# Kernel tuning notes

Hardware: AMD Instinct MI355X
Metric: run time of the kernel (lower is better)

## Reference

```python
import jax, jax.numpy as jnp
import numpy as np

R = 32  # voxel resolution

def leaky(x):
    return jnp.where(x > 0, x, 0.1 * x)

def bn(x, gamma, beta, axes, eps=1e-4):
    mu = jnp.mean(x, axis=axes, keepdims=True)
    var = jnp.var(x, axis=axes, keepdims=True)
    shape = [1] * x.ndim
    shape[1] = x.shape[1]
    g = gamma.reshape(shape)
    b = beta.reshape(shape)
    return (x - mu) * jax.lax.rsqrt(var + eps) * g + b

def voxelize(features, coords, r):
    # features: (B, C, N), coords: (B, 3, N)
    B, C, N = features.shape
    mean = jnp.mean(coords, axis=2, keepdims=True)
    norm = (coords - mean + 1.0) / 2.0 * r
    norm = jnp.clip(norm, 0.0, r - 1.0)            # (B, 3, N) continuous voxel coords
    vox = jnp.round(norm).astype(jnp.int32)
    flat = (vox[:, 0] * r + vox[:, 1]) * r + vox[:, 2]      # (B, N)
    seg = (flat + jnp.arange(B, dtype=jnp.int32)[:, None] * (r ** 3)).reshape(-1)
    data = features.transpose(0, 2, 1).reshape(B * N, C)
    sums = jax.ops.segment_sum(data, seg, num_segments=B * r ** 3)
    cnt = jax.ops.segment_sum(jnp.ones((B * N,), data.dtype), seg, num_segments=B * r ** 3)
    avg = sums / jnp.maximum(cnt, 1.0)[:, None]
    grid = avg.reshape(B, r, r, r, C).transpose(0, 4, 1, 2, 3)  # (B, C, r, r, r)
    return grid, norm

def trilinear_devoxelize(grid, norm, r):
    # grid: (B, C, r, r, r), norm: (B, 3, N) in [0, r-1]
    B, C = grid.shape[:2]
    N = norm.shape[2]
    lo = jnp.floor(norm).astype(jnp.int32)
    frac = norm - lo.astype(norm.dtype)
    hi = jnp.minimum(lo + 1, r - 1)
    gf = grid.reshape(B, C, r ** 3)
    out = jnp.zeros((B, C, N), grid.dtype)
    for dx in (0, 1):
        for dy in (0, 1):
            for dz in (0, 1):
                ix = hi[:, 0] if dx else lo[:, 0]
                iy = hi[:, 1] if dy else lo[:, 1]
                iz = hi[:, 2] if dz else lo[:, 2]
                wx = frac[:, 0] if dx else 1.0 - frac[:, 0]
                wy = frac[:, 1] if dy else 1.0 - frac[:, 1]
                wz = frac[:, 2] if dz else 1.0 - frac[:, 2]
                idx = (ix * r + iy) * r + iz                    # (B, N)
                g = jnp.take_along_axis(gf, idx[:, None, :], axis=2)  # (B, C, N)
                out = out + g * (wx * wy * wz)[:, None, :]
    return out

def conv3d(x, w, b):
    y = jax.lax.conv_general_dilated(
        x, w, window_strides=(1, 1, 1), padding=[(1, 1)] * 3,
        dimension_numbers=('NCDHW', 'OIDHW', 'NCDHW'))
    return y + b[None, :, None, None, None]

def setup_inputs() -> dict:
    key = jax.random.key(0)
    ks = jax.random.split(key, 8)
    B, Cin, Cout, N = 8, 64, 64, 32768
    s1 = 1.0 / np.sqrt(Cin * 27)
    s2 = 1.0 / np.sqrt(Cout * 27)
    return {
        'features': jax.random.normal(ks[0], (B, Cin, N), jnp.float32),
        'coords': jax.random.normal(ks[1], (B, 3, N), jnp.float32),
        'conv1_w': jax.random.normal(ks[2], (Cout, Cin, 3, 3, 3), jnp.float32) * s1,
        'conv1_b': jnp.zeros((Cout,), jnp.float32),
        'bn1_g': jnp.ones((Cout,), jnp.float32),
        'bn1_b': jnp.zeros((Cout,), jnp.float32),
        'conv2_w': jax.random.normal(ks[3], (Cout, Cout, 3, 3, 3), jnp.float32) * s2,
        'conv2_b': jnp.zeros((Cout,), jnp.float32),
        'bn2_g': jnp.ones((Cout,), jnp.float32),
        'bn2_b': jnp.zeros((Cout,), jnp.float32),
        'mlp_w': jax.random.normal(ks[4], (Cout, Cin), jnp.float32) / np.sqrt(Cin),
        'mlp_b': jnp.zeros((Cout,), jnp.float32),
        'bnp_g': jnp.ones((Cout,), jnp.float32),
        'bnp_b': jnp.zeros((Cout,), jnp.float32),
    }

def reference(features, coords, conv1_w, conv1_b, bn1_g, bn1_b,
              conv2_w, conv2_b, bn2_g, bn2_b, mlp_w, mlp_b, bnp_g, bnp_b):
    grid, norm = voxelize(features, coords, R)
    v = leaky(bn(conv3d(grid, conv1_w, conv1_b), bn1_g, bn1_b, (0, 2, 3, 4)))
    v = leaky(bn(conv3d(v, conv2_w, conv2_b), bn2_g, bn2_b, (0, 2, 3, 4)))
    sampled = trilinear_devoxelize(v, norm, R)                 # (B, Cout, N)
    p = jnp.einsum('oi,bin->bon', mlp_w, features) + mlp_b[None, :, None]
    p = leaky(bn(p, bnp_g, bnp_b, (0, 2)))
    fused = sampled + p
    return fused, v
```

## Files before the change

### kernel.cpp

```cpp
#include <hip/hip_runtime.h>
#include <hip/hip_bf16.h>

#define BB 8
#define CC 64
#define NPTS 32768
#define RR 32
#define RV 32768
#define MTOT (BB*RV)
#define EPSV 1e-4f

#define OFF_BUFA 0u
#define OFF_BUFB 16777216u
#define OFF_WB1  25165824u
#define OFF_WB2  25221120u
#define OFF_ZG   25276416u
#define OFF_BASE 25276480u
#define OFF_AUX  25800768u
#define OFF_CELL 25801024u
#define OFF_CNT  26063168u
#define OFF_MEAN 26325312u
#define OFF_PART1 26325504u
#define OFF_PART2 26456576u
#define OFF_SCL1 26587648u
#define OFF_SFT1 26587712u
#define OFF_SCL2 26587776u
#define OFF_SFT2 26587840u
#define OFF_WM   26587904u
#define OFF_PARTP 26590208u
#define OFF_SCLP 27114496u
#define OFF_SFTP 27114560u
#define OFF_NORM 33554432u

typedef __attribute__((ext_vector_type(8))) __bf16 bf16x8;
typedef __attribute__((ext_vector_type(8))) unsigned short u16x8;
typedef __attribute__((ext_vector_type(4))) float f32x4;

__device__ __forceinline__ float b2f(ushort u) {
    union { unsigned u; float f; } x; x.u = ((unsigned)u) << 16; return x.f;
}
__device__ __forceinline__ ushort f2b(float f) {
    __hip_bfloat16 h = __float2bfloat16(f);
    return *reinterpret_cast<ushort*>(&h);
}

__global__ void k_coord_mean(const float* __restrict__ coords, float* __restrict__ mean) {
    int ba = blockIdx.x >> 3, ch = blockIdx.x & 7;
    const float* src = coords + (size_t)ba * NPTS + ch * 4096;
    float s = 0.f;
    for (int i = threadIdx.x; i < 4096; i += 256) s += src[i];
    __shared__ float red[256];
    red[threadIdx.x] = s; __syncthreads();
    for (int w = 128; w > 0; w >>= 1) {
        if (threadIdx.x < w) red[threadIdx.x] += red[threadIdx.x + w];
        __syncthreads();
    }
    if (threadIdx.x == 0) atomicAdd(&mean[ba], red[0]);
}

__global__ void k_cellid(const float* __restrict__ coords, const float* __restrict__ mean,
                         float* __restrict__ norm, int* __restrict__ cellid,
                         unsigned* __restrict__ cnt) {
    int idx = blockIdx.x * 256 + threadIdx.x;
    int b = idx >> 15, n = idx & (NPTS - 1);
    int flat = 0;
    #pragma unroll
    for (int a = 0; a < 3; ++a) {
        float c = coords[((size_t)(b * 3 + a)) * NPTS + n];
        float nm = (c - mean[b * 3 + a] * (1.0f / NPTS) + 1.0f) * (0.5f * RR);
        nm = fminf(fmaxf(nm, 0.0f), (float)(RR - 1));
        norm[((size_t)(b * 3 + a)) * NPTS + n] = nm;
        flat = flat * RR + (int)rintf(nm);
    }
    int cell = b * RV + flat;
    cellid[idx] = cell;
    atomicAdd(&cnt[cell], 1u);
}

__global__ void k_scan1(const unsigned* __restrict__ cnt, unsigned* __restrict__ base,
                        unsigned* __restrict__ aux) {
    int tid = threadIdx.x;
    int c0 = blockIdx.x * 1024 + tid * 4;
    unsigned v0 = cnt[c0], v1 = cnt[c0 + 1], v2 = cnt[c0 + 2], v3 = cnt[c0 + 3];
    unsigned tot = v0 + v1 + v2 + v3;
    __shared__ unsigned sc[256];
    sc[tid] = tot; __syncthreads();
    for (int off = 1; off < 256; off <<= 1) {
        unsigned t = (tid >= off) ? sc[tid - off] : 0u;
        __syncthreads();
        sc[tid] += t;
        __syncthreads();
    }
    unsigned excl = sc[tid] - tot;
    base[c0] = excl;
    base[c0 + 1] = excl + v0;
    base[c0 + 2] = excl + v0 + v1;
    base[c0 + 3] = excl + v0 + v1 + v2;
    if (tid == 255) aux[blockIdx.x] = sc[255];
}

__global__ void k_scan2(unsigned* __restrict__ aux) {
    int tid = threadIdx.x;
    unsigned own = aux[tid];
    __shared__ unsigned sc[256];
    sc[tid] = own; __syncthreads();
    for (int off = 1; off < 256; off <<= 1) {
        unsigned t = (tid >= off) ? sc[tid - off] : 0u;
        __syncthreads();
        sc[tid] += t;
        __syncthreads();
    }
    aux[tid] = sc[tid] - own;
}

__global__ void k_scan3(unsigned* __restrict__ base, const unsigned* __restrict__ aux) {
    int i = blockIdx.x * 256 + threadIdx.x;
    base[i] += aux[i >> 10];
}

__global__ __launch_bounds__(256) void k_scatfeat(
    const float* __restrict__ feats, const int* __restrict__ cellid,
    unsigned* __restrict__ base, ushort* __restrict__ fsort,
    const ushort* __restrict__ wmb, const float* __restrict__ mbias,
    ushort* __restrict__ pb, float* __restrict__ partp) {
    __shared__ float t[64 * 65];
    __shared__ unsigned spos[64];
    __shared__ float sf[512];
    int b = blockIdx.x >> 9;
    int n0 = (blockIdx.x & 511) * 64;
    int tid = threadIdx.x;
    #pragma unroll
    for (int k = 0; k < 16; ++k) {
        int idx = k * 256 + tid;
        int c = idx >> 6, nl = idx & 63;
        t[c * 65 + nl] = feats[((size_t)(b * 64 + c)) * NPTS + n0 + nl];
    }
    if (tid < 64) {
        int cell = cellid[(b << 15) + n0 + tid];
        spos[tid] = atomicAdd(&base[cell], 1u);
    }
    __syncthreads();
    #pragma unroll
    for (int it = 0; it < 2; ++it) {
        int pl = it * 32 + (tid >> 3);
        int j = tid & 7;
        unsigned pos = spos[pl];
        u16x8 v;
        #pragma unroll
        for (int k = 0; k < 8; ++k) v[k] = f2b(t[(j * 8 + k) * 65 + pl]);
        *reinterpret_cast<u16x8*>(fsort + (((size_t)pos) << 6) + j * 8) = v;
    }
    int w = tid >> 6, l = tid & 63;
    int nl = l & 15, kg = l >> 4;
    bf16x8 Af[2];
    #pragma unroll
    for (int ks = 0; ks < 2; ++ks) {
        union { u16x8 u; bf16x8 h; } cv;
        #pragma unroll
        for (int j = 0; j < 8; ++j)
            cv.u[j] = f2b(t[(ks * 32 + kg * 8 + j) * 65 + w * 16 + nl]);
        Af[ks] = cv.h;
    }
    f32x4 acc[4];
    #pragma unroll
    for (int cb = 0; cb < 4; ++cb) acc[cb] = (f32x4){0.f, 0.f, 0.f, 0.f};
    #pragma unroll
    for (int ks = 0; ks < 2; ++ks)
        #pragma unroll
        for (int cb = 0; cb < 4; ++cb) {
            bf16x8 Bf = *reinterpret_cast<const bf16x8*>(wmb + (cb * 16 + nl) * 64 + ks * 32 + kg * 8);
            acc[cb] = __builtin_amdgcn_mfma_f32_16x16x32_bf16(Af[ks], Bf, acc[cb], 0, 0, 0);
        }
    float ss[4] = {0.f, 0.f, 0.f, 0.f}, qq[4] = {0.f, 0.f, 0.f, 0.f};
    #pragma unroll
    for (int cb = 0; cb < 4; ++cb) {
        float bsv = mbias[cb * 16 + nl];
        #pragma unroll
        for (int r = 0; r < 4; ++r) {
            float yv = acc[cb][r] + bsv;
            int pt = w * 16 + kg * 4 + r;
            pb[(((size_t)((b << 15) + n0 + pt)) << 6) + cb * 16 + nl] = f2b(yv);
            ss[cb] += yv; qq[cb] += yv * yv;
        }
    }
    #pragma unroll
    for (int cb = 0; cb < 4; ++cb) {
        ss[cb] += __shfl_xor(ss[cb], 16); ss[cb] += __shfl_xor(ss[cb], 32);
        qq[cb] += __shfl_xor(qq[cb], 16); qq[cb] += __shfl_xor(qq[cb], 32);
    }
    if (l < 16) {
        #pragma unroll
        for (int cb = 0; cb < 4; ++cb) {
            sf[w * 128 + cb * 16 + nl] = ss[cb];
            sf[w * 128 + 64 + cb * 16 + nl] = qq[cb];
        }
    }
    __syncthreads();
    if (tid < 128)
        partp[(size_t)tid * 4096 + blockIdx.x] =
            sf[tid] + sf[128 + tid] + sf[256 + tid] + sf[384 + tid];
}

__global__ __launch_bounds__(256) void k_gather(
    const ushort* __restrict__ fsort, const unsigned* __restrict__ base,
    const unsigned* __restrict__ cnt, __hip_bfloat16* __restrict__ xb) {
    int cell = blockIdx.x * 4 + (threadIdx.x >> 6);
    int lane = threadIdx.x & 63;
    unsigned n = cnt[cell];
    unsigned start = base[cell] - n;
    const ushort* rows = fsort + (((size_t)start) << 6) + lane;
    float acc = 0.f;
    unsigned i = 0;
    for (; i + 8 <= n; i += 8) {
        float f0 = b2f(rows[((size_t)(i + 0)) << 6]);
        float f1 = b2f(rows[((size_t)(i + 1)) << 6]);
        float f2 = b2f(rows[((size_t)(i + 2)) << 6]);
        float f3 = b2f(rows[((size_t)(i + 3)) << 6]);
        float f4 = b2f(rows[((size_t)(i + 4)) << 6]);
        float f5 = b2f(rows[((size_t)(i + 5)) << 6]);
        float f6 = b2f(rows[((size_t)(i + 6)) << 6]);
        float f7 = b2f(rows[((size_t)(i + 7)) << 6]);
        acc += ((f0 + f1) + (f2 + f3)) + ((f4 + f5) + (f6 + f7));
    }
    for (; i < n; ++i) acc += b2f(rows[((size_t)i) << 6]);
    float inv = (n > 0) ? (1.0f / (float)n) : 0.f;
    xb[((size_t)cell << 6) + lane] = __float2bfloat16(acc * inv);
}

__global__ void k_wb(const float* __restrict__ w, __hip_bfloat16* __restrict__ wb) {
    int i = blockIdx.x * 256 + threadIdx.x;
    if (i >= CC * CC * 27) return;
    int tap = i % 27, t = i / 27;
    int ci = t & 63, co = t >> 6;
    wb[((size_t)(tap * 64 + co)) * 64 + ci] = __float2bfloat16(w[i]);
}

__global__ void k_wm(const float* __restrict__ w, ushort* __restrict__ wmb) {
    int i = blockIdx.x * 256 + threadIdx.x;
    if (i < 4096) wmb[i] = f2b(w[i]);
}

template<int MODE>
__global__ __launch_bounds__(512, 2) void k_conv_mfma(
    const ushort* __restrict__ src, const ushort* __restrict__ wb,
    const float* __restrict__ bias, const float* __restrict__ scl,
    const float* __restrict__ sft, ushort* __restrict__ y,
    float* __restrict__ part, const ushort* __restrict__ zg) {
    __shared__ __align__(16) char sh[128000 + 32768];
    char* wsh = sh + 128000;
    int tid = threadIdx.x;
    int lane = tid & 63, wid = tid >> 6;
    int tile = ((blockIdx.x & 7) << 6) | (blockIdx.x >> 3);
    int twi = tile & 3, thi = (tile >> 2) & 3;
    int tdi = (tile >> 4) & 3, b = tile >> 6;
    int d0 = tdi * 8, h0 = thi * 8, w0 = twi * 8;

    auto stage_wgt = [&](int g) {
        const ushort* wgrp = wb + g * 8192;
        char* wdst0 = wsh + (g & 1) * 16384;
        #pragma unroll
        for (int i = 0; i < 2; ++i) {
            int idx = i * 8 + wid;
            int c = idx * 64 + lane;
            int row = c >> 3, off = c & 7;
            const ushort* gsrc = wgrp + (((row << 3) + (off ^ (row & 7))) << 3);
            char* ldst = wdst0 + (idx << 10);
            __builtin_amdgcn_global_load_lds(
                (const __attribute__((address_space(1))) void*)gsrc,
                (__attribute__((address_space(3))) void*)ldst, 16, 0, 0);
        }
    };

    float sc8[8], sf8[8];
    if (MODE == 1) {
        int c0 = (lane & 7) * 8;
        #pragma unroll
        for (int j = 0; j < 8; ++j) { sc8[j] = scl[c0 + j]; sf8[j] = sft[c0 + j]; }
    }

    #pragma unroll
    for (int it = 0; it < 16; ++it) {
        int idx = it * 8 + wid;
        if (idx < 125) {
            int c = idx * 64 + lane;
            int row = c >> 3, off = c & 7;
            int dz = row / 100, rem = row - dz * 100;
            int hz = rem / 10, wz = rem - hz * 10;
            int gd = d0 - 1 + dz, gh = h0 - 1 + hz, gw = w0 - 1 + wz;
            bool inb = ((unsigned)gd < 32u) && ((unsigned)gh < 32u) && ((unsigned)gw < 32u);
            if (MODE == 0) {
                int srcoff = off ^ (row & 7);
                const ushort* gsrc = inb
                    ? src + ((((size_t)((b << 15) | (gd << 10) | (gh << 5) | gw)) << 6) + srcoff * 8)
                    : zg;
                char* ldst = sh + (idx << 10);
                __builtin_amdgcn_global_load_lds(
                    (const __attribute__((address_space(1))) void*)gsrc,
                    (__attribute__((address_space(3))) void*)ldst, 16, 0, 0);
            } else {
                u16x8 v = {0, 0, 0, 0, 0, 0, 0, 0};
                if (inb) {
                    v = *reinterpret_cast<const u16x8*>(
                        src + ((((size_t)((b << 15) | (gd << 10) | (gh << 5) | gw)) << 6) + off * 8));
                    #pragma unroll
                    for (int j = 0; j < 8; ++j) {
                        float f = fmaf(b2f(v[j]), sc8[j], sf8[j]);
                        f = f > 0.f ? f : 0.1f * f;
                        v[j] = f2b(f);
                    }
                }
                int la = ((row << 7) + (off << 4)) ^ ((row & 7) << 4);
                *reinterpret_cast<u16x8*>(sh + la) = v;
            }
        }
    }
    stage_wgt(0);

    int nl = lane & 15, kg = lane >> 4;
    int rbase = wid * 100 + (nl >> 3) * 10 + (nl & 7);
    int bswz = (nl & 7) << 4;

    f32x4 acc[4][4];
    #pragma unroll
    for (int mi = 0; mi < 4; ++mi)
        #pragma unroll
        for (int cb = 0; cb < 4; ++cb) acc[mi][cb] = (f32x4){0.f, 0.f, 0.f, 0.f};

    __syncthreads();

    #pragma unroll 1
    for (int g = 0; g < 14; ++g) {
        if (g < 13) stage_wgt(g + 1);
        const char* wlds = wsh + (g & 1) * 16384;
        #pragma unroll
        for (int tl = 0; tl < 2; ++tl) {
            int t = g * 2 + tl;
            if (t < 27) {
                int kd = t / 9, rm = t - kd * 9;
                int kh = rm / 3, kw = rm - kh * 3;
                int rt = rbase + kd * 100 + kh * 10 + kw;
                bf16x8 a[4][2];
                #pragma unroll
                for (int mi = 0; mi < 4; ++mi) {
                    int r = rt + mi * 20;
                    int ba = ((r << 7) + (kg << 4)) ^ ((r & 7) << 4);
                    a[mi][0] = *reinterpret_cast<const bf16x8*>(sh + ba);
                    a[mi][1] = *reinterpret_cast<const bf16x8*>(sh + (ba ^ 64));
                }
                bf16x8 bf[4][2];
                #pragma unroll
                for (int cb = 0; cb < 4; ++cb) {
                    int rowb = tl * 64 + cb * 16 + nl;
                    int bb0 = ((rowb << 7) + (kg << 4)) ^ bswz;
                    bf[cb][0] = *reinterpret_cast<const bf16x8*>(wlds + bb0);
                    bf[cb][1] = *reinterpret_cast<const bf16x8*>(wlds + (bb0 ^ 64));
                }
                __builtin_amdgcn_s_setprio(1);
                #pragma unroll
                for (int ks = 0; ks < 2; ++ks)
                    #pragma unroll
                    for (int mi = 0; mi < 4; ++mi)
                        #pragma unroll
                        for (int cb = 0; cb < 4; ++cb)
                            acc[mi][cb] = __builtin_amdgcn_mfma_f32_16x16x32_bf16(
                                a[mi][ks], bf[cb][ks], acc[mi][cb], 0, 0, 0);
                __builtin_amdgcn_s_setprio(0);
            }
        }
        __syncthreads();
    }

    int d = d0 + wid;
    float bs[4];
    #pragma unroll
    for (int cb = 0; cb < 4; ++cb) bs[cb] = bias[cb * 16 + nl];
    float ss[4] = {0.f, 0.f, 0.f, 0.f}, qq[4] = {0.f, 0.f, 0.f, 0.f};
    #pragma unroll
    for (int mi = 0; mi < 4; ++mi) {
        int h = h0 + mi * 2 + (kg >> 1);
        int w = w0 + (kg & 1) * 4;
        size_t vox = (size_t)((b << 15) | (d << 10) | (h << 5) | w);
        #pragma unroll
        for (int cb = 0; cb < 4; ++cb) {
            int co = cb * 16 + nl;
            #pragma unroll
            for (int r = 0; r < 4; ++r) {
                float yv = acc[mi][cb][r] + bs[cb];
                y[((vox + r) << 6) + co] = f2b(yv);
                ss[cb] += yv; qq[cb] += yv * yv;
            }
        }
    }
    #pragma unroll
    for (int cb = 0; cb < 4; ++cb) {
        ss[cb] += __shfl_xor(ss[cb], 16); ss[cb] += __shfl_xor(ss[cb], 32);
        qq[cb] += __shfl_xor(qq[cb], 16); qq[cb] += __shfl_xor(qq[cb], 32);
    }
    float* sf2 = (float*)sh;
    __syncthreads();
    if (lane < 16) {
        #pragma unroll
        for (int cb = 0; cb < 4; ++cb) {
            sf2[wid * 128 + cb * 16 + nl] = ss[cb];
            sf2[wid * 128 + 64 + cb * 16 + nl] = qq[cb];
        }
    }
    __syncthreads();
    if (tid < 128) {
        float t = sf2[tid] + sf2[128 + tid] + sf2[256 + tid] + sf2[384 + tid]
                + sf2[512 + tid] + sf2[640 + tid] + sf2[768 + tid] + sf2[896 + tid];
        part[tid * 512 + blockIdx.x] = t;
    }
}

__global__ void k_redbn(const float* __restrict__ part, const float* __restrict__ g,
                        const float* __restrict__ bb, float* __restrict__ scl,
                        float* __restrict__ sft, int cnt) {
    int c = blockIdx.x;
    float s = 0.f, q = 0.f;
    for (int i = threadIdx.x; i < cnt; i += 256) {
        s += part[(size_t)c * cnt + i];
        q += part[(size_t)(64 + c) * cnt + i];
    }
    __shared__ float rs[256], rq[256];
    rs[threadIdx.x] = s; rq[threadIdx.x] = q; __syncthreads();
    for (int w = 128; w > 0; w >>= 1) {
        if (threadIdx.x < w) { rs[threadIdx.x] += rs[threadIdx.x + w]; rq[threadIdx.x] += rq[threadIdx.x + w]; }
        __syncthreads();
    }
    if (threadIdx.x == 0) {
        float mu = rs[0] * (1.0f / MTOT);
        float var = rq[0] * (1.0f / MTOT) - mu * mu;
        float sc = g[c] * rsqrtf(var + EPSV);
        scl[c] = sc; sft[c] = bb[c] - mu * sc;
    }
}

__global__ void k_transpose(const ushort* __restrict__ in, const float* __restrict__ scl,
                            const float* __restrict__ sft, float* __restrict__ out) {
    __shared__ float t[64 * 65];
    size_t base = (size_t)blockIdx.x * 4096;
    int gv0 = blockIdx.x * 64;
    int b = gv0 >> 15;
    int vox0 = gv0 & 32767;
    int chl = threadIdx.x & 63;
    float sc = scl[chl], sf = sft[chl];
    #pragma unroll
    for (int k = 0; k < 16; ++k) {
        int idx = k * 256 + threadIdx.x;
        float v = fmaf(b2f(in[base + idx]), sc, sf);
        t[(idx >> 6) * 65 + (idx & 63)] = v > 0.f ? v : 0.1f * v;
    }
    __syncthreads();
    #pragma unroll
    for (int k = 0; k < 16; ++k) {
        int idx = k * 256 + threadIdx.x;
        int ch = idx >> 6, voxl = idx & 63;
        out[((size_t)(b * 64 + ch)) * RV + vox0 + voxl] = t[voxl * 65 + ch];
    }
}

__global__ __launch_bounds__(256) void k_final(
    float* __restrict__ out, const ushort* __restrict__ pbuf,
    const ushort* __restrict__ vraw, const float* __restrict__ norm,
    const float* __restrict__ scl, const float* __restrict__ sft,
    const float* __restrict__ sclp, const float* __restrict__ sftp) {
    __shared__ float smp[64 * 65];
    int b = blockIdx.x >> 9;
    int n0 = (blockIdx.x & 511) * 64;
    int wid = threadIdx.x >> 6, lane = threadIdx.x & 63;
    const ushort* gb = vraw + (((size_t)b) << 15) * CC;
    const float* nrm0 = norm + ((size_t)(b * 3)) * NPTS;
    float sc = scl[lane], sf = sft[lane];
    float scp = sclp[lane], sfp = sftp[lane];

    #pragma unroll 2
    for (int i = 0; i < 16; ++i) {
        int pl = wid * 16 + i;
        int n = n0 + pl;
        float v0 = nrm0[n];
        float v1 = nrm0[NPTS + n];
        float v2 = nrm0[2 * NPTS + n];
        int lx = (int)floorf(v0), ly = (int)floorf(v1), lz = (int)floorf(v2);
        float fx = v0 - (float)lx, fy = v1 - (float)ly, fz = v2 - (float)lz;
        int hx = min(lx + 1, 31), hy = min(ly + 1, 31), hz = min(lz + 1, 31);
        float gx = 1.f - fx, gy = 1.f - fy, gz = 1.f - fz;

        int i000 = ((lx * 32 + ly) * 32 + lz) << 6;
        int i001 = ((lx * 32 + ly) * 32 + hz) << 6;
        int i010 = ((lx * 32 + hy) * 32 + lz) << 6;
        int i011 = ((lx * 32 + hy) * 32 + hz) << 6;
        int i100 = ((hx * 32 + ly) * 32 + lz) << 6;
        int i101 = ((hx * 32 + ly) * 32 + hz) << 6;
        int i110 = ((hx * 32 + hy) * 32 + lz) << 6;
        int i111 = ((hx * 32 + hy) * 32 + hz) << 6;

        float w000 = gx * gy * gz, w001 = gx * gy * fz;
        float w010 = gx * fy * gz, w011 = gx * fy * fz;
        float w100 = fx * gy * gz, w101 = fx * gy * fz;
        float w110 = fx * fy * gz, w111 = fx * fy * fz;

        float r0 = fmaf(b2f(gb[i000 + lane]), sc, sf); r0 = r0 > 0.f ? r0 : 0.1f * r0;
        float r1 = fmaf(b2f(gb[i001 + lane]), sc, sf); r1 = r1 > 0.f ? r1 : 0.1f * r1;
        float r2 = fmaf(b2f(gb[i010 + lane]), sc, sf); r2 = r2 > 0.f ? r2 : 0.1f * r2;
        float r3 = fmaf(b2f(gb[i011 + lane]), sc, sf); r3 = r3 > 0.f ? r3 : 0.1f * r3;
        float r4 = fmaf(b2f(gb[i100 + lane]), sc, sf); r4 = r4 > 0.f ? r4 : 0.1f * r4;
        float r5 = fmaf(b2f(gb[i101 + lane]), sc, sf); r5 = r5 > 0.f ? r5 : 0.1f * r5;
        float r6 = fmaf(b2f(gb[i110 + lane]), sc, sf); r6 = r6 > 0.f ? r6 : 0.1f * r6;
        float r7 = fmaf(b2f(gb[i111 + lane]), sc, sf); r7 = r7 > 0.f ? r7 : 0.1f * r7;

        float s = r0 * w000 + r1 * w001 + r2 * w010 + r3 * w011
                + r4 * w100 + r5 * w101 + r6 * w110 + r7 * w111;

        float pv = fmaf(b2f(pbuf[(((size_t)((b << 15) + n)) << 6) + lane]), scp, sfp);
        pv = pv > 0.f ? pv : 0.1f * pv;
        smp[pl * 65 + lane] = s + pv;
    }
    __syncthreads();

    #pragma unroll 4
    for (int i = 0; i < 16; ++i) {
        int co = i * 4 + wid;
        out[((size_t)(b * 64 + co)) * NPTS + n0 + lane] = smp[lane * 65 + co];
    }
}

extern "C" void kernel_launch(void* const* d_in, const int* in_sizes, int n_in,
                              void* d_out, int out_size, void* d_ws, size_t ws_size,
                              hipStream_t stream) {
    const float* features = (const float*)d_in[0];
    const float* coords   = (const float*)d_in[1];
    const float* conv1_w  = (const float*)d_in[2];
    const float* conv1_b  = (const float*)d_in[3];
    const float* bn1_g    = (const float*)d_in[4];
    const float* bn1_b    = (const float*)d_in[5];
    const float* conv2_w  = (const float*)d_in[6];
    const float* conv2_b  = (const float*)d_in[7];
    const float* bn2_g    = (const float*)d_in[8];
    const float* bn2_b    = (const float*)d_in[9];
    const float* mlp_w    = (const float*)d_in[10];
    const float* mlp_b    = (const float*)d_in[11];
    const float* bnp_g    = (const float*)d_in[12];
    const float* bnp_b    = (const float*)d_in[13];

    float* ws    = (float*)d_ws;
    ushort* fsort  = (ushort*)(ws + OFF_BUFA);
    ushort* y2b    = (ushort*)(ws + OFF_BUFA);
    __hip_bfloat16* xb  = (__hip_bfloat16*)(ws + OFF_BUFB);
    __hip_bfloat16* wb1 = (__hip_bfloat16*)(ws + OFF_WB1);
    __hip_bfloat16* wb2 = (__hip_bfloat16*)(ws + OFF_WB2);
    ushort* zg   = (ushort*)(ws + OFF_ZG);
    unsigned* base    = (unsigned*)(ws + OFF_BASE);
    unsigned* aux     = (unsigned*)(ws + OFF_AUX);
    int* cellid       = (int*)(ws + OFF_CELL);
    unsigned* cnt     = (unsigned*)(ws + OFF_CNT);
    float* mean  = ws + OFF_MEAN;
    float* part1 = ws + OFF_PART1;
    float* part2 = ws + OFF_PART2;
    float* scl1  = ws + OFF_SCL1;
    float* sft1  = ws + OFF_SFT1;
    float* scl2  = ws + OFF_SCL2;
    float* sft2  = ws + OFF_SFT2;
    ushort* wmb  = (ushort*)(ws + OFF_WM);
    float* partp = ws + OFF_PARTP;
    float* sclp  = ws + OFF_SCLP;
    float* sftp  = ws + OFF_SFTP;
    float* nrm   = ws + OFF_NORM;

    float* outF  = (float*)d_out;
    float* outV  = (float*)d_out + (size_t)16777216;
    ushort* y1b  = (ushort*)outV;
    ushort* pbuf = (ushort*)(outV + (size_t)8388608);

    hipMemsetAsync(cnt, 0, 262144 * 4, stream);
    hipMemsetAsync(zg, 0, 256, stream);
    hipMemsetAsync(mean, 0, 24 * 4, stream);

    k_coord_mean<<<192, 256, 0, stream>>>(coords, mean);
    k_cellid<<<1024, 256, 0, stream>>>(coords, mean, nrm, cellid, cnt);
    k_scan1<<<256, 256, 0, stream>>>(cnt, base, aux);
    k_scan2<<<1, 256, 0, stream>>>(aux);
    k_scan3<<<1024, 256, 0, stream>>>(base, aux);

    k_wb<<<432, 256, 0, stream>>>(conv1_w, wb1);
    k_wb<<<432, 256, 0, stream>>>(conv2_w, wb2);
    k_wm<<<16, 256, 0, stream>>>(mlp_w, wmb);

    k_scatfeat<<<4096, 256, 0, stream>>>(features, cellid, base, fsort,
                                         wmb, mlp_b, pbuf, partp);
    k_redbn<<<64, 256, 0, stream>>>(partp, bnp_g, bnp_b, sclp, sftp, 4096);
    k_gather<<<65536, 256, 0, stream>>>(fsort, base, cnt, xb);

    k_conv_mfma<0><<<512, 512, 0, stream>>>((const ushort*)xb, (const ushort*)wb1, conv1_b,
                                            nullptr, nullptr, y1b, part1, zg);
    k_redbn<<<64, 256, 0, stream>>>(part1, bn1_g, bn1_b, scl1, sft1, 512);

    k_conv_mfma<1><<<512, 512, 0, stream>>>(y1b, (const ushort*)wb2, conv2_b,
                                            scl1, sft1, y2b, part2, zg);
    k_redbn<<<64, 256, 0, stream>>>(part2, bn2_g, bn2_b, scl2, sft2, 512);

    k_final<<<4096, 256, 0, stream>>>(outF, pbuf, y2b, nrm, scl2, sft2, sclp, sftp);

    k_transpose<<<4096, 256, 0, stream>>>(y2b, scl2, sft2, outV);
}
```

Measured before the change: 363.8 us.

## Split conv input channels into two halves to halve LDS footprint

The conv kernel now runs two passes, each over 32 input channels, and the weight layout is reordered so each half is contiguous. Halo and weight staging buffers shrink to half their size, so two blocks can fit per CU instead of one. The launch-bounds hint is raised to match. In exchange, the halo is staged twice with extra barriers, and the tighter register budget may cause spills.

```diff
diff --git a/kernel.cpp b/kernel.cpp
--- a/kernel.cpp
+++ b/kernel.cpp
@@ -231,7 +231,8 @@
     if (i >= CC * CC * 27) return;
     int tap = i % 27, t = i / 27;
     int ci = t & 63, co = t >> 6;
-    wb[((size_t)(tap * 64 + co)) * 64 + ci] = __float2bfloat16(w[i]);
+    int half = ci >> 5;
+    wb[(((size_t)((half * 27 + tap) * 64 + co)) << 5) + (ci & 31)] = __float2bfloat16(w[i]);
 }
 
 __global__ void k_wm(const float* __restrict__ w, ushort* __restrict__ wmb) {
@@ -240,13 +241,13 @@
 }
 
 template<int MODE>
-__global__ __launch_bounds__(512, 2) void k_conv_mfma(
+__global__ __launch_bounds__(512, 4) void k_conv_mfma(
     const ushort* __restrict__ src, const ushort* __restrict__ wb,
     const float* __restrict__ bias, const float* __restrict__ scl,
     const float* __restrict__ sft, ushort* __restrict__ y,
     float* __restrict__ part, const ushort* __restrict__ zg) {
-    __shared__ __align__(16) char sh[128000 + 32768];
-    char* wsh = sh + 128000;
+    __shared__ __align__(16) char sh[64000 + 16384];
+    char* wsh = sh + 64000;
     int tid = threadIdx.x;
     int lane = tid & 63, wid = tid >> 6;
     int tile = ((blockIdx.x & 7) << 6) | (blockIdx.x >> 3);
@@ -254,70 +255,60 @@
     int tdi = (tile >> 4) & 3, b = tile >> 6;
     int d0 = tdi * 8, h0 = thi * 8, w0 = twi * 8;
 
-    auto stage_wgt = [&](int g) {
-        const ushort* wgrp = wb + g * 8192;
-        char* wdst0 = wsh + (g & 1) * 16384;
-        #pragma unroll
-        for (int i = 0; i < 2; ++i) {
-            int idx = i * 8 + wid;
-            int c = idx * 64 + lane;
-            int row = c >> 3, off = c & 7;
-            const ushort* gsrc = wgrp + (((row << 3) + (off ^ (row & 7))) << 3);
-            char* ldst = wdst0 + (idx << 10);
-            __builtin_amdgcn_global_load_lds(
-                (const __attribute__((address_space(1))) void*)gsrc,
-                (__attribute__((address_space(3))) void*)ldst, 16, 0, 0);
-        }
+    auto stage_wgt = [&](int half, int g) {
+        const ushort* wgrp = wb + (((half * 27 + g * 2)) << 11);
+        char* wdst = wsh + (g & 1) * 8192;
+        int c = (wid << 6) + lane;
+        int row = c >> 2, off = c & 3;
+        const ushort* gsrc = wgrp + (((row << 2) + (off ^ (row & 3))) << 3);
+        __builtin_amdgcn_global_load_lds(
+            (const __attribute__((address_space(1))) void*)gsrc,
+            (__attribute__((address_space(3))) void*)(wdst + (wid << 10)), 16, 0, 0);
     };
 
-    float sc8[8], sf8[8];
-    if (MODE == 1) {
-        int c0 = (lane & 7) * 8;
-        #pragma unroll
-        for (int j = 0; j < 8; ++j) { sc8[j] = scl[c0 + j]; sf8[j] = sft[c0 + j]; }
-    }
-
-    #pragma unroll
-    for (int it = 0; it < 16; ++it) {
-        int idx = it * 8 + wid;
-        if (idx < 125) {
-            int c = idx * 64 + lane;
-            int row = c >> 3, off = c & 7;
-            int dz = row / 100, rem = row - dz * 100;
-            int hz = rem / 10, wz = rem - hz * 10;
-            int gd = d0 - 1 + dz, gh = h0 - 1 + hz, gw = w0 - 1 + wz;
-            bool inb = ((unsigned)gd < 32u) && ((unsigned)gh < 32u) && ((unsigned)gw < 32u);
-            if (MODE == 0) {
-                int srcoff = off ^ (row & 7);
-                const ushort* gsrc = inb
-                    ? src + ((((size_t)((b << 15) | (gd << 10) | (gh << 5) | gw)) << 6) + srcoff * 8)
-                    : zg;
-                char* ldst = sh + (idx << 10);
-                __builtin_amdgcn_global_load_lds(
-                    (const __attribute__((address_space(1))) void*)gsrc,
-                    (__attribute__((address_space(3))) void*)ldst, 16, 0, 0);
-            } else {
-                u16x8 v = {0, 0, 0, 0, 0, 0, 0, 0};
-                if (inb) {
-                    v = *reinterpret_cast<const u16x8*>(
-                        src + ((((size_t)((b << 15) | (gd << 10) | (gh << 5) | gw)) << 6) + off * 8));
-                    #pragma unroll
-                    for (int j = 0; j < 8; ++j) {
-                        float f = fmaf(b2f(v[j]), sc8[j], sf8[j]);
-                        f = f > 0.f ? f : 0.1f * f;
-                        v[j] = f2b(f);
+    auto stage_halo = [&](int half) {
+        float sc8[8], sf8[8];
+        if (MODE == 1) {
+            int c0 = half * 32 + (lane & 3) * 8;
+            #pragma unroll
+            for (int j = 0; j < 8; ++j) { sc8[j] = scl[c0 + j]; sf8[j] = sft[c0 + j]; }
+        }
+        #pragma unroll
+        for (int it = 0; it < 8; ++it) {
+            int idx = it * 8 + wid;
+            int c = (idx << 6) + lane;
+            if (c < 4000) {
+                int row = c >> 2, off = c & 3;
+                int dz = row / 100, rem = row - dz * 100;
+                int hz = rem / 10, wz = rem - hz * 10;
+                int gd = d0 - 1 + dz, gh = h0 - 1 + hz, gw = w0 - 1 + wz;
+                bool inb = ((unsigned)gd < 32u) && ((unsigned)gh < 32u) && ((unsigned)gw < 32u);
+                size_t vbase = (((size_t)((b << 15) | (gd << 10) | (gh << 5) | gw)) << 6) + half * 32;
+                if (MODE == 0) {
+                    int soff = off ^ (row & 3);
+                    const ushort* gsrc = inb ? src + vbase + soff * 8 : zg;
+                    __builtin_amdgcn_global_load_lds(
+                        (const __attribute__((address_space(1))) void*)gsrc,
+                        (__attribute__((address_space(3))) void*)(sh + (idx << 10)), 16, 0, 0);
+                } else {
+                    u16x8 v = {0, 0, 0, 0, 0, 0, 0, 0};
+                    if (inb) {
+                        v = *reinterpret_cast<const u16x8*>(src + vbase + off * 8);
+                        #pragma unroll
+                        for (int j = 0; j < 8; ++j) {
+                            float f = fmaf(b2f(v[j]), sc8[j], sf8[j]);
+                            f = f > 0.f ? f : 0.1f * f;
+                            v[j] = f2b(f);
+                        }
                     }
+                    *reinterpret_cast<u16x8*>(sh + (row << 6) + ((off ^ (row & 3)) << 4)) = v;
                 }
-                int la = ((row << 7) + (off << 4)) ^ ((row & 7) << 4);
-                *reinterpret_cast<u16x8*>(sh + la) = v;
             }
         }
-    }
-    stage_wgt(0);
+    };
 
     int nl = lane & 15, kg = lane >> 4;
     int rbase = wid * 100 + (nl >> 3) * 10 + (nl & 7);
-    int bswz = (nl & 7) << 4;
 
     f32x4 acc[4][4];
     #pragma unroll
@@ -325,12 +316,8 @@
         #pragma unroll
         for (int cb = 0; cb < 4; ++cb) acc[mi][cb] = (f32x4){0.f, 0.f, 0.f, 0.f};
 
-    __syncthreads();
-
-    #pragma unroll 1
-    for (int g = 0; g < 14; ++g) {
-        if (g < 13) stage_wgt(g + 1);
-        const char* wlds = wsh + (g & 1) * 16384;
+    auto compute = [&](int g) {
+        const char* wlds = wsh + (g & 1) * 8192;
         #pragma unroll
         for (int tl = 0; tl < 2; ++tl) {
             int t = g * 2 + tl;
@@ -338,34 +325,48 @@
                 int kd = t / 9, rm = t - kd * 9;
                 int kh = rm / 3, kw = rm - kh * 3;
                 int rt = rbase + kd * 100 + kh * 10 + kw;
-                bf16x8 a[4][2];
+                bf16x8 a[4];
                 #pragma unroll
                 for (int mi = 0; mi < 4; ++mi) {
                     int r = rt + mi * 20;
-                    int ba = ((r << 7) + (kg << 4)) ^ ((r & 7) << 4);
-                    a[mi][0] = *reinterpret_cast<const bf16x8*>(sh + ba);
-                    a[mi][1] = *reinterpret_cast<const bf16x8*>(sh + (ba ^ 64));
+                    a[mi] = *reinterpret_cast<const bf16x8*>(
+                        sh + (r << 6) + ((kg ^ (r & 3)) << 4));
                 }
-                bf16x8 bf[4][2];
+                bf16x8 bf[4];
                 #pragma unroll
                 for (int cb = 0; cb < 4; ++cb) {
                     int rowb = tl * 64 + cb * 16 + nl;
-                    int bb0 = ((rowb << 7) + (kg << 4)) ^ bswz;
-                    bf[cb][0] = *reinterpret_cast<const bf16x8*>(wlds + bb0);
-                    bf[cb][1] = *reinterpret_cast<const bf16x8*>(wlds + (bb0 ^ 64));
+                    bf[cb] = *reinterpret_cast<const bf16x8*>(
+                        wlds + (rowb << 6) + ((kg ^ (rowb & 3)) << 4));
                 }
                 __builtin_amdgcn_s_setprio(1);
                 #pragma unroll
-                for (int ks = 0; ks < 2; ++ks)
+                for (int mi = 0; mi < 4; ++mi)
                     #pragma unroll
-                    for (int mi = 0; mi < 4; ++mi)
-                        #pragma unroll
-                        for (int cb = 0; cb < 4; ++cb)
-                            acc[mi][cb] = __builtin_amdgcn_mfma_f32_16x16x32_bf16(
-                                a[mi][ks], bf[cb][ks], acc[mi][cb], 0, 0, 0);
+                    for (int cb = 0; cb < 4; ++cb)
+                        acc[mi][cb] = __builtin_amdgcn_mfma_f32_16x16x32_bf16(
+                            a[mi], bf[cb], acc[mi][cb], 0, 0, 0);
                 __builtin_amdgcn_s_setprio(0);
             }
         }
+    };
+
+    stage_halo(0);
+    stage_wgt(0, 0);
+    __syncthreads();
+    #pragma unroll 1
+    for (int g = 0; g < 14; ++g) {
+        if (g < 13) stage_wgt(0, g + 1);
+        compute(g);
+        __syncthreads();
+    }
+    stage_halo(1);
+    stage_wgt(1, 0);
+    __syncthreads();
+    #pragma unroll 1
+    for (int g = 0; g < 14; ++g) {
+        if (g < 13) stage_wgt(1, g + 1);
+        compute(g);
         __syncthreads();
     }
 
```

Result: no change. 357.8 us (-1.6%).
